# Optimization experiments

Hardware: AMD Instinct MI355X
Metric: run time of the kernel (lower is better)

Reference implementation:

```python
import jax, jax.numpy as jnp
import numpy as np

N = 50000      # nodes
E = 800000     # edges (before self-loops)
IN = 128       # in_channels
HID = 32       # hidden_channels
H = 4          # heads (hidden layers)
H_LAST = 6     # heads of final conv (concat=False -> mean)
OUT = 2        # out_channels
NEG = 0.2      # LeakyReLU slope in GATConv


def setup_inputs() -> dict:
    key = jax.random.key(0)
    ks = jax.random.split(key, 24)
    r = lambda k, s, sc=0.1: (jax.random.normal(k, s, jnp.float32) * sc)
    inp = {
        "x": jax.random.normal(ks[0], (N, IN), jnp.float32),
        "edge_index": jax.random.randint(ks[1], (2, E), 0, N, dtype=jnp.int32),
        "edge_attr": jax.random.normal(ks[2], (E, 1), jnp.float32),  # ignored by GATConv (edge_dim=None)
        # layer 0: GATConv(IN -> HID, heads=H, concat) + Linear(IN -> HID*H)
        "c0_W": r(ks[3], (IN, H * HID)), "c0_as": r(ks[4], (H, HID)), "c0_ad": r(ks[5], (H, HID)), "c0_b": jnp.zeros((H * HID,), jnp.float32),
        "l0_W": r(ks[6], (IN, H * HID)), "l0_b": jnp.zeros((H * HID,), jnp.float32),
        # layer 1 (middle): GATConv(HID*H -> HID, heads=H) + Linear(HID*H -> HID*H)
        "c1_W": r(ks[7], (H * HID, H * HID)), "c1_as": r(ks[8], (H, HID)), "c1_ad": r(ks[9], (H, HID)), "c1_b": jnp.zeros((H * HID,), jnp.float32),
        "l1_W": r(ks[10], (H * HID, H * HID)), "l1_b": jnp.zeros((H * HID,), jnp.float32),
        # layer 2 (last): GATConv(HID*H -> OUT, heads=H_LAST, concat=False) + Linear(HID*H -> OUT)
        "c2_W": r(ks[11], (H * HID, H_LAST * OUT)), "c2_as": r(ks[12], (H_LAST, OUT)), "c2_ad": r(ks[13], (H_LAST, OUT)), "c2_b": jnp.zeros((OUT,), jnp.float32),
        "l2_W": r(ks[14], (H * HID, OUT)), "l2_b": jnp.zeros((OUT,), jnp.float32),
    }
    return inp


def gat_conv(x, src, dst, W, a_src, a_dst, b, heads, ch, concat):
    n = x.shape[0]
    xw = (x @ W).reshape(n, heads, ch)                      # [N,H,C]
    al_s = jnp.einsum('nhc,hc->nh', xw, a_src)              # [N,H]
    al_d = jnp.einsum('nhc,hc->nh', xw, a_dst)
    alpha = jax.nn.leaky_relu(al_s[src] + al_d[dst], NEG)   # [E,H]
    # segment softmax over edges sharing the same destination node
    m = jax.ops.segment_max(alpha, dst, num_segments=n)
    e = jnp.exp(alpha - m[dst])
    s = jax.ops.segment_sum(e, dst, num_segments=n)
    coef = e / s[dst]                                       # [E,H]
    out = jax.ops.segment_sum(xw[src] * coef[:, :, None], dst, num_segments=n)  # [N,H,C]
    out = out.reshape(n, heads * ch) if concat else out.mean(axis=1)
    return out + b


def reference(x, edge_index, edge_attr,
              c0_W, c0_as, c0_ad, c0_b, l0_W, l0_b,
              c1_W, c1_as, c1_ad, c1_b, l1_W, l1_b,
              c2_W, c2_as, c2_ad, c2_b, l2_W, l2_b):
    n = x.shape[0]
    loops = jnp.arange(n, dtype=edge_index.dtype)  # GATConv add_self_loops=True
    src = jnp.concatenate([edge_index[0], loops])
    dst = jnp.concatenate([edge_index[1], loops])
    # edge_attr is ignored: GATConv built without edge_dim has lin_edge=None
    h = jax.nn.relu(gat_conv(x, src, dst, c0_W, c0_as, c0_ad, c0_b, H, HID, True) + x @ l0_W + l0_b)
    h = jax.nn.relu(gat_conv(h, src, dst, c1_W, c1_as, c1_ad, c1_b, H, HID, True) + h @ l1_W + l1_b)
    out = gat_conv(h, src, dst, c2_W, c2_as, c2_ad, c2_b, H_LAST, OUT, False) + h @ l2_W + l2_b
    return out
```

## Files before the change

kernel.cpp:

```cpp
#include <hip/hip_runtime.h>
#include <hip/hip_bf16.h>


#define NEG_SLOPE 0.2f
#define SC_CHUNK 4096
#define CAP 64

typedef __attribute__((ext_vector_type(8))) short short8;
typedef __attribute__((ext_vector_type(4))) float floatx4;

static __device__ __forceinline__ float leaky(float x) {
    return x > 0.f ? x : NEG_SLOPE * x;
}

static __device__ __forceinline__ unsigned short f2bf(float f) {
    unsigned int u = __float_as_uint(f);
    u = (u + 0x7fffu + ((u >> 16) & 1u)) >> 16;
    return (unsigned short)u;
}

static __device__ __forceinline__ unsigned int pack_bf2(float lo, float hi) {
    return (unsigned int)f2bf(lo) | ((unsigned int)f2bf(hi) << 16);
}

static __device__ __forceinline__ float bflo(unsigned int u) {
    return __uint_as_float(u << 16);
}
static __device__ __forceinline__ float bfhi(unsigned int u) {
    return __uint_as_float(u & 0xffff0000u);
}

static __device__ __forceinline__ short8 frag_from_f32(const float* p) {
    float4 f0 = ((const float4*)p)[0];
    float4 f1 = ((const float4*)p)[1];
    short8 r;
    r[0] = (short)f2bf(f0.x); r[1] = (short)f2bf(f0.y);
    r[2] = (short)f2bf(f0.z); r[3] = (short)f2bf(f0.w);
    r[4] = (short)f2bf(f1.x); r[5] = (short)f2bf(f1.y);
    r[6] = (short)f2bf(f1.z); r[7] = (short)f2bf(f1.w);
    return r;
}

__global__ __launch_bounds__(256) void k_bucket(
    const int* __restrict__ ei, int E, int N, int rs,
    int* __restrict__ cnt, unsigned short* __restrict__ col,
    const float* __restrict__ W0, unsigned short* __restrict__ T0,
    const float* __restrict__ W1, unsigned short* __restrict__ T1,
    const float* __restrict__ W2, unsigned short* __restrict__ T2,
    const float* __restrict__ W3, unsigned short* __restrict__ T3,
    const float* __restrict__ c2W, const float* __restrict__ l2W,
    unsigned short* __restrict__ WT5) {
    if (blockIdx.y == gridDim.y - 1) {
        int tid = blockIdx.x * 256 + threadIdx.x;
        for (int j = tid; j < 65536; j += 2048) {
            int wsel = j >> 14, t = j & 16383;
            int n = t >> 7, k = t & 127;
            const float* W = (wsel == 0) ? W0 : (wsel == 1) ? W1 : (wsel == 2) ? W2 : W3;
            unsigned short* T = (wsel == 0) ? T0 : (wsel == 1) ? T1 : (wsel == 2) ? T2 : T3;
            T[n * 128 + k] = f2bf(W[k * 128 + n]);
        }
        {
            int n = tid >> 7, k = tid & 127;
            float v = 0.f;
            if (n < 12) v = c2W[k * 12 + n];
            else if (n < 14) v = l2W[k * 2 + (n - 12)];
            WT5[n * 128 + k] = f2bf(v);
        }
        return;
    }
    int lo = blockIdx.x * rs, hi = lo + rs;
    int base = blockIdx.y * SC_CHUNK;
    int ET = E + N;
#pragma unroll 4
    for (int o = threadIdx.x; o < SC_CHUNK; o += 256) {
        int e = base + o;
        if (e >= ET) break;
        int d = (e < E) ? ei[E + e] : (e - E);
        if (d < lo || d >= hi) continue;
        int s = (e < E) ? ei[e] : d;
        int pos = atomicAdd(&cnt[d], 1);
        if (pos < CAP) col[(d << 6) + pos] = (unsigned short)s;
    }
}

__global__ __launch_bounds__(256) void k_gemm_mfma(
    const float* __restrict__ x0,
    const unsigned short* __restrict__ Ab,
    const unsigned short* __restrict__ W1T,
    unsigned int* __restrict__ XWb,
    const float* __restrict__ a_s, const float* __restrict__ a_d,
    float4* __restrict__ ALS4, float4* __restrict__ ALD4,
    const unsigned short* __restrict__ W2T,
    const float* __restrict__ b2,
    unsigned short* __restrict__ Hsb,
    int M) {
    __shared__ short8 Wl[128 * 17];
    int which = blockIdx.y;
    const short8* W8 = (const short8*)(which ? W2T : W1T);

    for (int u = threadIdx.x; u < 2048; u += 256)
        Wl[(u >> 4) * 17 + (u & 15)] = W8[u];

    int w = threadIdx.x >> 6, lane = threadIdx.x & 63;
    int m = lane & 15, q = lane >> 4;
    const short8* A8 = (const short8*)Ab;

    short8 af[2][4];
    int rt0 = blockIdx.x * 8 + w;
#pragma unroll
    for (int t = 0; t < 2; t++) {
        int arow = (rt0 + t * 4) * 16 + m;
        int lrow = (arow < M) ? arow : (M - 1);
#pragma unroll
        for (int ks = 0; ks < 4; ks++) {
            af[t][ks] = x0 ? frag_from_f32(x0 + (size_t)lrow * 128 + (ks * 4 + q) * 8)
                           : A8[arow * 16 + ks * 4 + q];
        }
    }
    __syncthreads();

#pragma unroll
    for (int t = 0; t < 2; t++) {
        floatx4 acc[8];
#pragma unroll
        for (int ct = 0; ct < 8; ct++) acc[ct] = (floatx4){0.f, 0.f, 0.f, 0.f};
#pragma unroll
        for (int ks = 0; ks < 4; ks++) {
#pragma unroll
            for (int ct = 0; ct < 8; ct++) {
                short8 bfrag = Wl[(ct * 16 + m) * 17 + ks * 4 + q];
                acc[ct] = __builtin_amdgcn_mfma_f32_16x16x32_bf16(af[t][ks], bfrag, acc[ct], 0, 0, 0);
            }
        }

        int crow0 = (rt0 + t * 4) * 16 + q * 4;
        if (which) {
#pragma unroll
            for (int ct = 0; ct < 8; ct++) {
                int gc = ct * 16 + m;
                float bias = b2[gc];
#pragma unroll
                for (int r = 0; r < 4; r++) {
                    int gr = crow0 + r;
                    if (gr < M) Hsb[gr * 128 + gc] = f2bf(acc[ct][r] + bias);
                }
            }
        } else {
#pragma unroll
            for (int ct = 0; ct < 4; ct++) {
#pragma unroll
                for (int r = 0; r < 4; r++) {
                    int gr = crow0 + r;
                    if (gr < M)
                        XWb[gr * 64 + ct * 16 + m] = pack_bf2(acc[ct][r], acc[ct + 4][r]);
                }
            }
            float sv[4][4], dv[4][4];
#pragma unroll
            for (int h = 0; h < 4; h++) {
                float as0 = a_s[h * 32 + m], as1 = a_s[h * 32 + 16 + m];
                float ad0 = a_d[h * 32 + m], ad1 = a_d[h * 32 + 16 + m];
#pragma unroll
                for (int r = 0; r < 4; r++) {
                    sv[h][r] = acc[2 * h][r] * as0 + acc[2 * h + 1][r] * as1;
                    dv[h][r] = acc[2 * h][r] * ad0 + acc[2 * h + 1][r] * ad1;
                }
            }
#pragma unroll
            for (int off = 8; off >= 1; off >>= 1) {
#pragma unroll
                for (int h = 0; h < 4; h++)
#pragma unroll
                    for (int r = 0; r < 4; r++) {
                        sv[h][r] += __shfl_xor(sv[h][r], off);
                        dv[h][r] += __shfl_xor(dv[h][r], off);
                    }
            }
            if (m == 0) {
#pragma unroll
                for (int r = 0; r < 4; r++) {
                    int gr = crow0 + r;
                    if (gr < M) {
                        ALS4[gr] = make_float4(sv[0][r], sv[1][r], sv[2][r], sv[3][r]);
                        ALD4[gr] = make_float4(dv[0][r], dv[1][r], dv[2][r], dv[3][r]);
                    }
                }
            }
        }
    }
}

__global__ __launch_bounds__(256) void k_gemm_small(
    const unsigned short* __restrict__ Ab,
    const unsigned short* __restrict__ WT5,
    const float* __restrict__ c2as, const float* __restrict__ c2ad,
    const float* __restrict__ l2b,
    float* __restrict__ L2D, float* __restrict__ ALD2,
    float* __restrict__ out, int M) {
    int w = threadIdx.x >> 6, lane = threadIdx.x & 63;
    int m = lane & 15, q = lane >> 4;
    const short8* A8 = (const short8*)Ab;
    const short8* W8 = (const short8*)WT5;
    floatx4 acc = (floatx4){0.f, 0.f, 0.f, 0.f};
    int arow = blockIdx.x * 64 + w * 16 + m;
#pragma unroll
    for (int ks = 0; ks < 4; ks++) {
        short8 afrag = A8[arow * 16 + ks * 4 + q];
        short8 bfrag = W8[m * 16 + ks * 4 + q];
        acc = __builtin_amdgcn_mfma_f32_16x16x32_bf16(afrag, bfrag, acc, 0, 0, 0);
    }
    float asm_ = (m < 12) ? c2as[m] : 0.f;
    float adm  = (m < 12) ? c2ad[m] : 0.f;
    int crow0 = blockIdx.x * 64 + w * 16 + q * 4;
    float sc[4], dc[4];
#pragma unroll
    for (int r = 0; r < 4; r++) {
        sc[r] = acc[r] * asm_;
        dc[r] = acc[r] * adm;
    }
#pragma unroll
    for (int r = 0; r < 4; r++) {
        sc[r] += __shfl_xor(sc[r], 1);
        dc[r] += __shfl_xor(dc[r], 1);
    }
#pragma unroll
    for (int r = 0; r < 4; r++) {
        int gr = crow0 + r;
        if (gr >= M) continue;
        if (m < 12) {
            L2D[gr * 20 + m] = acc[r];
            if ((m & 1) == 0) {
                int h = m >> 1;
                L2D[gr * 20 + 12 + h] = sc[r];
                ALD2[gr * 8 + h] = dc[r];
            }
        } else if (m == 12) {
            out[gr * 2 + 0] = acc[r] + l2b[0];
        } else if (m == 13) {
            out[gr * 2 + 1] = acc[r] + l2b[1];
        }
    }
}

__global__ __launch_bounds__(256) void k_agg4(
    const int* __restrict__ cntv, const unsigned short* __restrict__ col,
    const uint4* __restrict__ XWb4,
    const float4* __restrict__ ALS4, const float4* __restrict__ ALD4,
    const float* __restrict__ cb,
    const unsigned short* __restrict__ Hsb, unsigned short* __restrict__ Hb, int N) {
    int wid = threadIdx.x >> 6, lane = threadIdx.x & 63;
    int node = blockIdx.x * 4 + wid;
    if (node >= N) return;
    int deg = cntv[node];
    if (deg > CAP) deg = CAP;
    int start = node << 6;
    int gq = lane >> 4, g = lane & 15;
    int hA = g >> 3;
    int cval = col[start + lane];
    float4 cl = ((const float4*)cb)[g];
    float4 ch = ((const float4*)cb)[g + 16];
    uint2 skl = ((const uint2*)(Hsb + node * 128))[g];
    uint2 skh = ((const uint2*)(Hsb + node * 128 + 64))[g];
    float4 ad = ALD4[node];
    float adA = hA ? ad.y : ad.x;
    float adB = hA ? ad.w : ad.z;

    float a0 = 0.f, a1 = 0.f, a2 = 0.f, a3 = 0.f;
    float b0 = 0.f, b1 = 0.f, b2 = 0.f, b3 = 0.f;
    float sA = 0.f, sB = 0.f;

#define QUAD(qq)                                                        \
    bool t##qq; float4 as##qq; uint4 u##qq;                             \
    {                                                                   \
        int idx = (qq) * 4 + gq;                                        \
        t##qq = idx < deg;                                              \
        int sv = __shfl(cval, t##qq ? idx : 0);                         \
        as##qq = ALS4[sv];                                              \
        u##qq = XWb4[(size_t)sv * 16 + g];                              \
    }

#define CQ(qq)                                                          \
    {                                                                   \
        float eA = t##qq ? __expf(leaky((hA ? as##qq.y : as##qq.x) + adA)) : 0.f; \
        float eB = t##qq ? __expf(leaky((hA ? as##qq.w : as##qq.z) + adB)) : 0.f; \
        sA += eA; sB += eB;                                             \
        a0 += eA * bflo(u##qq.x); b0 += eB * bfhi(u##qq.x);             \
        a1 += eA * bflo(u##qq.y); b1 += eB * bfhi(u##qq.y);             \
        a2 += eA * bflo(u##qq.z); b2 += eB * bfhi(u##qq.z);             \
        a3 += eA * bflo(u##qq.w); b3 += eB * bfhi(u##qq.w);             \
    }

    if (deg <= 16) {
        QUAD(0) QUAD(1) QUAD(2) QUAD(3)
        CQ(0) CQ(1) CQ(2) CQ(3)
    } else if (deg <= 24) {
        QUAD(0) QUAD(1) QUAD(2) QUAD(3) QUAD(4) QUAD(5)
        CQ(0) CQ(1) CQ(2) CQ(3) CQ(4) CQ(5)
    } else {
        QUAD(0) QUAD(1) QUAD(2) QUAD(3) QUAD(4) QUAD(5) QUAD(6) QUAD(7)
        CQ(0) CQ(1) CQ(2) CQ(3) CQ(4) CQ(5) CQ(6) CQ(7)
        for (int i = 32; i < deg; i += 4) {
            int idx = i + gq;
            bool tt = idx < deg;
            int sv = __shfl(cval, tt ? idx : 0);
            float4 as = ALS4[sv];
            uint4 uu = XWb4[(size_t)sv * 16 + g];
            float eA = tt ? __expf(leaky((hA ? as.y : as.x) + adA)) : 0.f;
            float eB = tt ? __expf(leaky((hA ? as.w : as.z) + adB)) : 0.f;
            sA += eA; sB += eB;
            a0 += eA * bflo(uu.x); b0 += eB * bfhi(uu.x);
            a1 += eA * bflo(uu.y); b1 += eB * bfhi(uu.y);
            a2 += eA * bflo(uu.z); b2 += eB * bfhi(uu.z);
            a3 += eA * bflo(uu.w); b3 += eB * bfhi(uu.w);
        }
    }
#undef QUAD
#undef CQ

#define RED2(v) { v += __shfl_xor(v, 16); v += __shfl_xor(v, 32); }
    RED2(sA) RED2(sB)
    RED2(a0) RED2(a1) RED2(a2) RED2(a3)
    RED2(b0) RED2(b1) RED2(b2) RED2(b3)
#undef RED2

    if (gq == 0) {
        float invA = 1.f / sA, invB = 1.f / sB;
        float v0 = a0 * invA + cl.x + bflo(skl.x);
        float v1 = a1 * invA + cl.y + bfhi(skl.x);
        float v2 = a2 * invA + cl.z + bflo(skl.y);
        float v3 = a3 * invA + cl.w + bfhi(skl.y);
        float w0 = b0 * invB + ch.x + bflo(skh.x);
        float w1 = b1 * invB + ch.y + bfhi(skh.x);
        float w2 = b2 * invB + ch.z + bflo(skh.y);
        float w3 = b3 * invB + ch.w + bfhi(skh.y);
        v0 = v0 > 0.f ? v0 : 0.f;  v1 = v1 > 0.f ? v1 : 0.f;
        v2 = v2 > 0.f ? v2 : 0.f;  v3 = v3 > 0.f ? v3 : 0.f;
        w0 = w0 > 0.f ? w0 : 0.f;  w1 = w1 > 0.f ? w1 : 0.f;
        w2 = w2 > 0.f ? w2 : 0.f;  w3 = w3 > 0.f ? w3 : 0.f;
        uint2 ol, oh;
        ol.x = pack_bf2(v0, v1); ol.y = pack_bf2(v2, v3);
        oh.x = pack_bf2(w0, w1); oh.y = pack_bf2(w2, w3);
        ((uint2*)(Hb + node * 128))[g] = ol;
        ((uint2*)(Hb + node * 128 + 64))[g] = oh;
    }
}

__global__ __launch_bounds__(256) void k_agg2(
    const int* __restrict__ cntv, const unsigned short* __restrict__ col,
    const float4* __restrict__ L2D4,
    const float* __restrict__ ALD2,
    const float* __restrict__ c2b,
    float* __restrict__ out, int N) {
    int g = threadIdx.x >> 4, l = threadIdx.x & 15;
    int node = blockIdx.x * 16 + g;
    if (node >= N) return;
    int deg = cntv[node];
    if (deg > CAP) deg = CAP;
    int start = node << 6;

    float m0 = (l      < deg) ? 1.f : 0.f;
    float m1 = (l + 16 < deg) ? 1.f : 0.f;
    float m2 = (l + 32 < deg) ? 1.f : 0.f;
    float m3 = (l + 48 < deg) ? 1.f : 0.f;
    int s0 = col[start + ((l      < deg) ? l      : 0)];
    int s1 = col[start + ((l + 16 < deg) ? l + 16 : 0)];
    int s2 = col[start + ((l + 32 < deg) ? l + 32 : 0)];
    int s3 = col[start + ((l + 48 < deg) ? l + 48 : 0)];

    float ald[6];
    {
        float4 d03 = *(const float4*)(ALD2 + node * 8);
        float2 d45 = *(const float2*)(ALD2 + node * 8 + 4);
        ald[0] = d03.x; ald[1] = d03.y; ald[2] = d03.z; ald[3] = d03.w;
        ald[4] = d45.x; ald[5] = d45.y;
    }

#define LOADN(k, sv)                                                       \
    float4 xA##k = L2D4[(size_t)(sv) * 5 + 0];                             \
    float4 xB##k = L2D4[(size_t)(sv) * 5 + 1];                             \
    float4 xC##k = L2D4[(size_t)(sv) * 5 + 2];                             \
    float4 aS##k = L2D4[(size_t)(sv) * 5 + 3];                             \
    float4 aT##k = L2D4[(size_t)(sv) * 5 + 4];
    LOADN(0, s0) LOADN(1, s1) LOADN(2, s2) LOADN(3, s3)
#undef LOADN

    float se[6], a0[6], a1[6];
#pragma unroll
    for (int h = 0; h < 6; h++) { se[h] = 0.f; a0[h] = 0.f; a1[h] = 0.f; }

#define COMPN(k, mk)                                                       \
    {                                                                      \
        float als[6] = {aS##k.x, aS##k.y, aS##k.z, aS##k.w, aT##k.x, aT##k.y}; \
        float xw[12] = {xA##k.x, xA##k.y, xA##k.z, xA##k.w,                \
                        xB##k.x, xB##k.y, xB##k.z, xB##k.w,                \
                        xC##k.x, xC##k.y, xC##k.z, xC##k.w};               \
        _Pragma("unroll")                                                  \
        for (int h = 0; h < 6; h++) {                                      \
            float e = (mk) * __expf(leaky(als[h] + ald[h]));               \
            se[h] += e;                                                    \
            a0[h] += e * xw[2 * h];                                        \
            a1[h] += e * xw[2 * h + 1];                                    \
        }                                                                  \
    }
    COMPN(0, m0) COMPN(1, m1) COMPN(2, m2) COMPN(3, m3)
#undef COMPN

#pragma unroll
    for (int m = 8; m >= 1; m >>= 1) {
#pragma unroll
        for (int h = 0; h < 6; h++) {
            se[h] += __shfl_xor(se[h], m);
            a0[h] += __shfl_xor(a0[h], m);
            a1[h] += __shfl_xor(a1[h], m);
        }
    }
    if (l == 0) {
        float o0 = 0.f, o1 = 0.f;
#pragma unroll
        for (int h = 0; h < 6; h++) {
            float inv = 1.f / se[h];
            o0 += a0[h] * inv;
            o1 += a1[h] * inv;
        }
        out[node * 2 + 0] += o0 * (1.f / 6.f) + c2b[0];
        out[node * 2 + 1] += o1 * (1.f / 6.f) + c2b[1];
    }
}


extern "C" void kernel_launch(void* const* d_in, const int* in_sizes, int n_in,
                              void* d_out, int out_size, void* d_ws, size_t ws_size,
                              hipStream_t stream) {
    const float* x   = (const float*)d_in[0];
    const int* ei    = (const int*)d_in[1];
    const float* c0W = (const float*)d_in[3];
    const float* c0as = (const float*)d_in[4];
    const float* c0ad = (const float*)d_in[5];
    const float* c0b = (const float*)d_in[6];
    const float* l0W = (const float*)d_in[7];
    const float* l0b = (const float*)d_in[8];
    const float* c1W = (const float*)d_in[9];
    const float* c1as = (const float*)d_in[10];
    const float* c1ad = (const float*)d_in[11];
    const float* c1b = (const float*)d_in[12];
    const float* l1W = (const float*)d_in[13];
    const float* l1b = (const float*)d_in[14];
    const float* c2W = (const float*)d_in[15];
    const float* c2as = (const float*)d_in[16];
    const float* c2ad = (const float*)d_in[17];
    const float* c2b = (const float*)d_in[18];
    const float* l2W = (const float*)d_in[19];
    const float* l2b = (const float*)d_in[20];
    float* out = (float*)d_out;

    const int N = in_sizes[0] / 128;
    const int E = in_sizes[1] / 2;
    const int ET = E + N;
    const int Mpad = (N + 63) & ~63;

    char* p = (char*)d_ws;
    auto alloc = [&](size_t bytes) -> void* {
        void* r = (void*)p;
        p += (bytes + 255) & ~(size_t)255;
        return r;
    };
    unsigned short* Hsb = (unsigned short*)alloc((size_t)N * 128 * 2);
    unsigned int* XWb = (unsigned int*)alloc((size_t)N * 64 * 4);
    unsigned short* Ab = (unsigned short*)alloc((size_t)Mpad * 128 * 2);
    unsigned short* W1T = (unsigned short*)alloc(128 * 128 * 2);
    unsigned short* W2T = (unsigned short*)alloc(128 * 128 * 2);
    unsigned short* W3T = (unsigned short*)alloc(128 * 128 * 2);
    unsigned short* W4T = (unsigned short*)alloc(128 * 128 * 2);
    unsigned short* WT5 = (unsigned short*)alloc(16 * 128 * 2);
    float* ALS = (float*)alloc((size_t)N * 4 * 4);
    float* ALD = (float*)alloc((size_t)N * 8 * 4);
    float* L2D = (float*)alloc((size_t)N * 20 * 4);
    int* cnt    = (int*)alloc((size_t)N * 4);
    unsigned short* col = (unsigned short*)alloc((size_t)N * CAP * 2);

    hipMemsetAsync(cnt, 0, (size_t)N * 4, stream);
    int rs = (N + 7) / 8;
    int chunks = (ET + SC_CHUNK - 1) / SC_CHUNK;
    dim3 bgrid(8, chunks + 1);
    k_bucket<<<bgrid, 256, 0, stream>>>(ei, E, N, rs, cnt, col,
                                        c0W, W1T, l0W, W2T, c1W, W3T, l1W, W4T,
                                        c2W, l2W, WT5);

    dim3 ggrid((Mpad + 127) / 128, 2);
    int nwb = (N + 3) / 4;

    k_gemm_mfma<<<ggrid, 256, 0, stream>>>(x, Ab, W1T, XWb, c0as, c0ad,
                                           (float4*)ALS, (float4*)ALD,
                                           W2T, l0b, Hsb, N);
    k_agg4<<<nwb, 256, 0, stream>>>(cnt, col, (const uint4*)XWb,
                                    (const float4*)ALS, (const float4*)ALD,
                                    c0b, Hsb, Ab, N);

    k_gemm_mfma<<<ggrid, 256, 0, stream>>>(nullptr, Ab, W3T, XWb, c1as, c1ad,
                                           (float4*)ALS, (float4*)ALD,
                                           W4T, l1b, Hsb, N);
    k_agg4<<<nwb, 256, 0, stream>>>(cnt, col, (const uint4*)XWb,
                                    (const float4*)ALS, (const float4*)ALD,
                                    c1b, Hsb, Ab, N);

    k_gemm_small<<<Mpad / 64, 256, 0, stream>>>(Ab, WT5, c2as, c2ad, l2b,
                                                L2D, ALD, out, N);
    k_agg2<<<(N + 15) / 16, 256, 0, stream>>>(cnt, col, (const float4*)L2D,
                                              ALD, c2b, out, N);
}
```

Measured before the change: 308.1 us.

## Pre-convert input to bf16 in bucket kernel and fuse dual GEMMs per block

The fp32-to-bf16 conversion of x moves into extra blocks of the bucketing kernel, writing a padded bf16 buffer, so the first GEMM no longer converts on the fly. The two-way GEMM grid (conv weights and linear weights in separate blocks) becomes one block that loads its A fragments once and runs both products, reloading the shared-memory weights in between. This halves the A-matrix reads and the block count per layer, at the cost of a second shared-memory weight load and an extra bf16 copy of x in the preprocessing pass. A second activation buffer is added so the layer inputs don't alias.

```diff
diff --git a/kernel.cpp b/kernel.cpp
--- a/kernel.cpp
+++ b/kernel.cpp
@@ -5,6 +5,7 @@
 #define NEG_SLOPE 0.2f
 #define SC_CHUNK 4096
 #define CAP 64
+#define XCROWS 16
 
 typedef __attribute__((ext_vector_type(8))) short short8;
 typedef __attribute__((ext_vector_type(4))) float floatx4;
@@ -30,27 +31,18 @@
     return __uint_as_float(u & 0xffff0000u);
 }
 
-static __device__ __forceinline__ short8 frag_from_f32(const float* p) {
-    float4 f0 = ((const float4*)p)[0];
-    float4 f1 = ((const float4*)p)[1];
-    short8 r;
-    r[0] = (short)f2bf(f0.x); r[1] = (short)f2bf(f0.y);
-    r[2] = (short)f2bf(f0.z); r[3] = (short)f2bf(f0.w);
-    r[4] = (short)f2bf(f1.x); r[5] = (short)f2bf(f1.y);
-    r[6] = (short)f2bf(f1.z); r[7] = (short)f2bf(f1.w);
-    return r;
-}
-
 __global__ __launch_bounds__(256) void k_bucket(
-    const int* __restrict__ ei, int E, int N, int rs,
+    const int* __restrict__ ei, int E, int N, int rs, int chunks,
     int* __restrict__ cnt, unsigned short* __restrict__ col,
     const float* __restrict__ W0, unsigned short* __restrict__ T0,
     const float* __restrict__ W1, unsigned short* __restrict__ T1,
     const float* __restrict__ W2, unsigned short* __restrict__ T2,
     const float* __restrict__ W3, unsigned short* __restrict__ T3,
     const float* __restrict__ c2W, const float* __restrict__ l2W,
-    unsigned short* __restrict__ WT5) {
-    if (blockIdx.y == gridDim.y - 1) {
+    unsigned short* __restrict__ WT5,
+    const float* __restrict__ x, unsigned short* __restrict__ Ab0, int Mpad) {
+    int y = blockIdx.y;
+    if (y == chunks) {
         int tid = blockIdx.x * 256 + threadIdx.x;
         for (int j = tid; j < 65536; j += 2048) {
             int wsel = j >> 14, t = j & 16383;
@@ -68,8 +60,28 @@
         }
         return;
     }
+    if (y > chunks) {
+        int bid = (y - chunks - 1) * 8 + blockIdx.x;
+        int tid = bid * 256 + threadIdx.x;
+        int total = Mpad * 32;
+        int nvalid = N * 32;
+        const float4* x4 = (const float4*)x;
+        ushort4* o4 = (ushort4*)Ab0;
+        for (int i = tid; i < total; i += XCROWS * 8 * 256) {
+            ushort4 o;
+            if (i < nvalid) {
+                float4 v = x4[i];
+                o.x = f2bf(v.x); o.y = f2bf(v.y);
+                o.z = f2bf(v.z); o.w = f2bf(v.w);
+            } else {
+                o.x = 0; o.y = 0; o.z = 0; o.w = 0;
+            }
+            o4[i] = o;
+        }
+        return;
+    }
     int lo = blockIdx.x * rs, hi = lo + rs;
-    int base = blockIdx.y * SC_CHUNK;
+    int base = y * SC_CHUNK;
     int ET = E + N;
 #pragma unroll 4
     for (int o = threadIdx.x; o < SC_CHUNK; o += 256) {
@@ -83,39 +95,32 @@
     }
 }
 
-__global__ __launch_bounds__(256) void k_gemm_mfma(
-    const float* __restrict__ x0,
+__global__ __launch_bounds__(256) void k_gemm2(
     const unsigned short* __restrict__ Ab,
-    const unsigned short* __restrict__ W1T,
+    const unsigned short* __restrict__ WcT,
+    const unsigned short* __restrict__ WlT,
     unsigned int* __restrict__ XWb,
     const float* __restrict__ a_s, const float* __restrict__ a_d,
     float4* __restrict__ ALS4, float4* __restrict__ ALD4,
-    const unsigned short* __restrict__ W2T,
-    const float* __restrict__ b2,
+    const float* __restrict__ lb,
     unsigned short* __restrict__ Hsb,
     int M) {
     __shared__ short8 Wl[128 * 17];
-    int which = blockIdx.y;
-    const short8* W8 = (const short8*)(which ? W2T : W1T);
-
-    for (int u = threadIdx.x; u < 2048; u += 256)
-        Wl[(u >> 4) * 17 + (u & 15)] = W8[u];
-
     int w = threadIdx.x >> 6, lane = threadIdx.x & 63;
     int m = lane & 15, q = lane >> 4;
     const short8* A8 = (const short8*)Ab;
 
+    for (int u = threadIdx.x; u < 2048; u += 256)
+        Wl[(u >> 4) * 17 + (u & 15)] = ((const short8*)WcT)[u];
+
     short8 af[2][4];
     int rt0 = blockIdx.x * 8 + w;
 #pragma unroll
     for (int t = 0; t < 2; t++) {
         int arow = (rt0 + t * 4) * 16 + m;
-        int lrow = (arow < M) ? arow : (M - 1);
-#pragma unroll
-        for (int ks = 0; ks < 4; ks++) {
-            af[t][ks] = x0 ? frag_from_f32(x0 + (size_t)lrow * 128 + (ks * 4 + q) * 8)
-                           : A8[arow * 16 + ks * 4 + q];
-        }
+#pragma unroll
+        for (int ks = 0; ks < 4; ks++)
+            af[t][ks] = A8[arow * 16 + ks * 4 + q];
     }
     __syncthreads();
 
@@ -132,59 +137,76 @@
                 acc[ct] = __builtin_amdgcn_mfma_f32_16x16x32_bf16(af[t][ks], bfrag, acc[ct], 0, 0, 0);
             }
         }
-
         int crow0 = (rt0 + t * 4) * 16 + q * 4;
-        if (which) {
+#pragma unroll
+        for (int ct = 0; ct < 4; ct++) {
+#pragma unroll
+            for (int r = 0; r < 4; r++) {
+                int gr = crow0 + r;
+                if (gr < M)
+                    XWb[gr * 64 + ct * 16 + m] = pack_bf2(acc[ct][r], acc[ct + 4][r]);
+            }
+        }
+        float sv[4][4], dv[4][4];
+#pragma unroll
+        for (int h = 0; h < 4; h++) {
+            float as0 = a_s[h * 32 + m], as1 = a_s[h * 32 + 16 + m];
+            float ad0 = a_d[h * 32 + m], ad1 = a_d[h * 32 + 16 + m];
+#pragma unroll
+            for (int r = 0; r < 4; r++) {
+                sv[h][r] = acc[2 * h][r] * as0 + acc[2 * h + 1][r] * as1;
+                dv[h][r] = acc[2 * h][r] * ad0 + acc[2 * h + 1][r] * ad1;
+            }
+        }
+#pragma unroll
+        for (int off = 8; off >= 1; off >>= 1) {
+#pragma unroll
+            for (int h = 0; h < 4; h++)
+#pragma unroll
+                for (int r = 0; r < 4; r++) {
+                    sv[h][r] += __shfl_xor(sv[h][r], off);
+                    dv[h][r] += __shfl_xor(dv[h][r], off);
+                }
+        }
+        if (m == 0) {
+#pragma unroll
+            for (int r = 0; r < 4; r++) {
+                int gr = crow0 + r;
+                if (gr < M) {
+                    ALS4[gr] = make_float4(sv[0][r], sv[1][r], sv[2][r], sv[3][r]);
+                    ALD4[gr] = make_float4(dv[0][r], dv[1][r], dv[2][r], dv[3][r]);
+                }
+            }
+        }
+    }
+
+    __syncthreads();
+    for (int u = threadIdx.x; u < 2048; u += 256)
+        Wl[(u >> 4) * 17 + (u & 15)] = ((const short8*)WlT)[u];
+    __syncthreads();
+
+#pragma unroll
+    for (int t = 0; t < 2; t++) {
+        floatx4 acc[8];
+#pragma unroll
+        for (int ct = 0; ct < 8; ct++) acc[ct] = (floatx4){0.f, 0.f, 0.f, 0.f};
+#pragma unroll
+        for (int ks = 0; ks < 4; ks++) {
 #pragma unroll
             for (int ct = 0; ct < 8; ct++) {
-                int gc = ct * 16 + m;
-                float bias = b2[gc];
-#pragma unroll
-                for (int r = 0; r < 4; r++) {
-                    int gr = crow0 + r;
-                    if (gr < M) Hsb[gr * 128 + gc] = f2bf(acc[ct][r] + bias);
-                }
-            }
-        } else {
-#pragma unroll
-            for (int ct = 0; ct < 4; ct++) {
-#pragma unroll
-                for (int r = 0; r < 4; r++) {
-                    int gr = crow0 + r;
-                    if (gr < M)
-                        XWb[gr * 64 + ct * 16 + m] = pack_bf2(acc[ct][r], acc[ct + 4][r]);
-                }
-            }
-            float sv[4][4], dv[4][4];
-#pragma unroll
-            for (int h = 0; h < 4; h++) {
-                float as0 = a_s[h * 32 + m], as1 = a_s[h * 32 + 16 + m];
-                float ad0 = a_d[h * 32 + m], ad1 = a_d[h * 32 + 16 + m];
-#pragma unroll
-                for (int r = 0; r < 4; r++) {
-                    sv[h][r] = acc[2 * h][r] * as0 + acc[2 * h + 1][r] * as1;
-                    dv[h][r] = acc[2 * h][r] * ad0 + acc[2 * h + 1][r] * ad1;
-                }
-            }
-#pragma unroll
-            for (int off = 8; off >= 1; off >>= 1) {
-#pragma unroll
-                for (int h = 0; h < 4; h++)
-#pragma unroll
-                    for (int r = 0; r < 4; r++) {
-                        sv[h][r] += __shfl_xor(sv[h][r], off);
-                        dv[h][r] += __shfl_xor(dv[h][r], off);
-                    }
-            }
-            if (m == 0) {
-#pragma unroll
-                for (int r = 0; r < 4; r++) {
-                    int gr = crow0 + r;
-                    if (gr < M) {
-                        ALS4[gr] = make_float4(sv[0][r], sv[1][r], sv[2][r], sv[3][r]);
-                        ALD4[gr] = make_float4(dv[0][r], dv[1][r], dv[2][r], dv[3][r]);
-                    }
-                }
+                short8 bfrag = Wl[(ct * 16 + m) * 17 + ks * 4 + q];
+                acc[ct] = __builtin_amdgcn_mfma_f32_16x16x32_bf16(af[t][ks], bfrag, acc[ct], 0, 0, 0);
+            }
+        }
+        int crow0 = (rt0 + t * 4) * 16 + q * 4;
+#pragma unroll
+        for (int ct = 0; ct < 8; ct++) {
+            int gc = ct * 16 + m;
+            float bias = lb[gc];
+#pragma unroll
+            for (int r = 0; r < 4; r++) {
+                int gr = crow0 + r;
+                if (gr < M) Hsb[gr * 128 + gc] = f2bf(acc[ct][r] + bias);
             }
         }
     }
@@ -465,8 +487,9 @@
         return r;
     };
     unsigned short* Hsb = (unsigned short*)alloc((size_t)N * 128 * 2);
-    unsigned int* XWb = (unsigned int*)alloc((size_t)N * 64 * 4);
-    unsigned short* Ab = (unsigned short*)alloc((size_t)Mpad * 128 * 2);
+    unsigned int* XWb  = (unsigned int*)alloc((size_t)N * 64 * 4);
+    unsigned short* Ab0 = (unsigned short*)alloc((size_t)Mpad * 128 * 2);
+    unsigned short* AbH = (unsigned short*)alloc((size_t)Mpad * 128 * 2);
     unsigned short* W1T = (unsigned short*)alloc(128 * 128 * 2);
     unsigned short* W2T = (unsigned short*)alloc(128 * 128 * 2);
     unsigned short* W3T = (unsigned short*)alloc(128 * 128 * 2);
@@ -481,29 +504,27 @@
     hipMemsetAsync(cnt, 0, (size_t)N * 4, stream);
     int rs = (N + 7) / 8;
     int chunks = (ET + SC_CHUNK - 1) / SC_CHUNK;
-    dim3 bgrid(8, chunks + 1);
-    k_bucket<<<bgrid, 256, 0, stream>>>(ei, E, N, rs, cnt, col,
+    dim3 bgrid(8, chunks + 1 + XCROWS);
+    k_bucket<<<bgrid, 256, 0, stream>>>(ei, E, N, rs, chunks, cnt, col,
                                         c0W, W1T, l0W, W2T, c1W, W3T, l1W, W4T,
-                                        c2W, l2W, WT5);
-
-    dim3 ggrid((Mpad + 127) / 128, 2);
+                                        c2W, l2W, WT5, x, Ab0, Mpad);
+
+    int gx = (Mpad + 127) / 128;
     int nwb = (N + 3) / 4;
 
-    k_gemm_mfma<<<ggrid, 256, 0, stream>>>(x, Ab, W1T, XWb, c0as, c0ad,
-                                           (float4*)ALS, (float4*)ALD,
-                                           W2T, l0b, Hsb, N);
+    k_gemm2<<<gx, 256, 0, stream>>>(Ab0, W1T, W2T, XWb, c0as, c0ad,
+                                    (float4*)ALS, (float4*)ALD, l0b, Hsb, N);
     k_agg4<<<nwb, 256, 0, stream>>>(cnt, col, (const uint4*)XWb,
                                     (const float4*)ALS, (const float4*)ALD,
-                                    c0b, Hsb, Ab, N);
-
-    k_gemm_mfma<<<ggrid, 256, 0, stream>>>(nullptr, Ab, W3T, XWb, c1as, c1ad,
-                                           (float4*)ALS, (float4*)ALD,
-                                           W4T, l1b, Hsb, N);
+                                    c0b, Hsb, AbH, N);
+
+    k_gemm2<<<gx, 256, 0, stream>>>(AbH, W3T, W4T, XWb, c1as, c1ad,
+                                    (float4*)ALS, (float4*)ALD, l1b, Hsb, N);
     k_agg4<<<nwb, 256, 0, stream>>>(cnt, col, (const uint4*)XWb,
                                     (const float4*)ALS, (const float4*)ALD,
-                                    c1b, Hsb, Ab, N);
-
-    k_gemm_small<<<Mpad / 64, 256, 0, stream>>>(Ab, WT5, c2as, c2ad, l2b,
+                                    c1b, Hsb, Ab0, N);
+
+    k_gemm_small<<<Mpad / 64, 256, 0, stream>>>(Ab0, WT5, c2as, c2ad, l2b,
                                                 L2D, ALD, out, N);
     k_agg2<<<(N + 15) / 16, 256, 0, stream>>>(cnt, col, (const float4*)L2D,
                                               ALD, c2b, out, N);
```

New measurement: 297.5 us. 3.5% less time.
